# Performance work log

Hardware: AMD Instinct MI355X
Metric: run time of the kernel (lower is better)

Reference implementation:

```python
import jax, jax.numpy as jnp
import numpy as np

B, L, T, D, H, DH = 8, 1024, 1024, 768, 12, 64
SPATIAL_DIM = 5


def setup_inputs() -> dict:
    key = jax.random.key(0)
    ks = jax.random.split(key, 12)
    scale = 1.0 / np.sqrt(D)
    inp = {
        "q": jax.random.normal(ks[0], (B, L, D), dtype=jnp.float32),
        "k": jax.random.normal(ks[1], (B, T, D), dtype=jnp.float32),
        "v": jax.random.normal(ks[2], (B, T, D), dtype=jnp.float32),
        "pairwise_locs": jax.random.normal(ks[3], (B, L, T, SPATIAL_DIM), dtype=jnp.float32),
        # last 64 key positions are padding in every batch row (never all-True)
        "key_padding_mask": jnp.broadcast_to(jnp.arange(T) >= T - 64, (B, T)),
        "Wq": jax.random.normal(ks[4], (D, H * DH), dtype=jnp.float32) * scale,
        "bq": jnp.zeros((H * DH,), dtype=jnp.float32),
        "Wk": jax.random.normal(ks[5], (D, H * DH), dtype=jnp.float32) * scale,
        "bk": jnp.zeros((H * DH,), dtype=jnp.float32),
        "Wv": jax.random.normal(ks[6], (D, H * DH), dtype=jnp.float32) * scale,
        "bv": jnp.zeros((H * DH,), dtype=jnp.float32),
        "Wo": jax.random.normal(ks[7], (H * DH, D), dtype=jnp.float32) * scale,
        "bo": jnp.zeros((D,), dtype=jnp.float32),
    }
    return inp


def reference(q, k, v, pairwise_locs, key_padding_mask, Wq, bq, Wk, bk, Wv, bv, Wo, bo):
    # pairwise_locs is accepted but unused in this forward path (as in the source).
    b, l, _ = q.shape
    t = k.shape[1]
    qh = (q @ Wq + bq).reshape(b, l, H, DH)  # b l h d
    kh = (k @ Wk + bk).reshape(b, t, H, DH)  # b t h d
    vh = (v @ Wv + bv).reshape(b, t, H, DH)  # b t h d
    attn = jnp.einsum('blhd,bthd->bhlt', qh, kh) / jnp.sqrt(jnp.float32(DH))
    attn = jnp.where(key_padding_mask[:, None, None, :], -jnp.inf, attn)
    fused_attn = jax.nn.softmax(attn, axis=-1)
    out = jnp.einsum('bhlt,bthd->blhd', fused_attn, vh).reshape(b, l, H * DH)
    return out @ Wo + bo  # dropout is identity in eval mode
```

## Files before the change

kernel.cpp:

```cpp
#include <hip/hip_runtime.h>
#include <hip/hip_bf16.h>
#include <cstdint>
#include <cstddef>

#define NB 8
#define NL 1024
#define NT 1024
#define ND 768
#define NH 12
#define NDH 64
#define NM (NB*NL)

typedef short short8 __attribute__((ext_vector_type(8)));
typedef unsigned short ushort4v __attribute__((ext_vector_type(4)));
typedef unsigned int uint4v __attribute__((ext_vector_type(4)));
typedef float f32x4 __attribute__((ext_vector_type(4)));
typedef float float4v __attribute__((ext_vector_type(4)));

__device__ __forceinline__ unsigned short f2bf(float f) {
  union { __hip_bfloat16 h; unsigned short u; } cv;
  cv.h = __float2bfloat16(f);
  return cv.u;
}
__device__ __forceinline__ unsigned pk2(float lo, float hi) {
  return (unsigned)f2bf(lo) | ((unsigned)f2bf(hi) << 16);
}
__device__ __forceinline__ void gll16(const void* g, void* l) {
  __builtin_amdgcn_global_load_lds(
      (const __attribute__((address_space(1))) unsigned int*)g,
      (__attribute__((address_space(3))) unsigned int*)l, 16, 0, 0);
}

__global__ __launch_bounds__(256) void cvt_kernel(
    const float* __restrict__ q, const float* __restrict__ k,
    const float* __restrict__ v, unsigned short* __restrict__ qb,
    unsigned short* __restrict__ kb, unsigned short* __restrict__ vb) {
  const float* src = blockIdx.y == 0 ? q : blockIdx.y == 1 ? k : v;
  unsigned short* dst = blockIdx.y == 0 ? qb : blockIdx.y == 1 ? kb : vb;
  size_t i = ((size_t)blockIdx.x * 256 + threadIdx.x) * 8;
  float4v x0 = *(const float4v*)&src[i];
  float4v x1 = *(const float4v*)&src[i + 4];
  uint4v y = {pk2(x0[0], x0[1]), pk2(x0[2], x0[3]),
              pk2(x1[0], x1[1]), pk2(x1[2], x1[3])};
  *(uint4v*)&dst[i] = y;
}

__global__ __launch_bounds__(256) void wt_kernel(
    const float* __restrict__ W0, const float* __restrict__ W1,
    const float* __restrict__ W2, const float* __restrict__ W3,
    unsigned short* __restrict__ Wt) {
  __shared__ float tile[32][33];
  const float* W = blockIdx.z == 0 ? W0 : blockIdx.z == 1 ? W1 : blockIdx.z == 2 ? W2 : W3;
  const int k0 = blockIdx.x * 32, n0 = blockIdx.y * 32;
  const int tx = threadIdx.x & 31, ty = threadIdx.x >> 5;
  for (int r = ty; r < 32; r += 8) tile[r][tx] = W[(size_t)(k0 + r) * ND + n0 + tx];
  __syncthreads();
  unsigned short* out = Wt + (size_t)blockIdx.z * ND * ND;
  for (int r = ty; r < 32; r += 8) out[(size_t)(n0 + r) * ND + k0 + tx] = f2bf(tile[tx][r]);
}

template<int MODE>
__global__ __launch_bounds__(256) void gemm_kernel(
    const unsigned short* __restrict__ A0, const unsigned short* __restrict__ A1,
    const unsigned short* __restrict__ Wt,
    const float* __restrict__ bias0, const float* __restrict__ bias1,
    unsigned short* __restrict__ outb0, unsigned short* __restrict__ outb1,
    float* __restrict__ outf) {
  __shared__ __align__(16) unsigned short As[128 * 64];
  __shared__ __align__(16) unsigned short Bs[128 * 64];
  const int tid = threadIdx.x, lane = tid & 63, w = tid >> 6;
  const int c = lane & 15, g = lane >> 4;
  const int wrow = w & 1, wcol = w >> 1;
  const int l8 = lane >> 3, l7 = lane & 7, csw = l7 ^ l8;
  const int mbase = blockIdx.x * 128, nbase = blockIdx.y * 128;
  const int z = (MODE == 0) ? blockIdx.z : MODE;

  const unsigned short* A = (MODE == 0) ? (z == 0 ? A0 : A1) : A0;
  const unsigned short* Bt = Wt + (size_t)z * ND * ND;
  const float* bias = (MODE == 0) ? (z == 0 ? bias0 : bias1) : bias0;

  f32x4 acc[4][4];
#pragma unroll
  for (int m = 0; m < 4; m++)
#pragma unroll
    for (int n = 0; n < 4; n++) acc[m][n] = (f32x4){0.f, 0.f, 0.f, 0.f};

  for (int k0 = 0; k0 < ND; k0 += 64) {
#pragma unroll
    for (int it = 0; it < 4; it++) {
      int r = it * 32 + w * 8 + l8;
      gll16(&A[(size_t)(mbase + r) * ND + k0 + csw * 8], &As[(it * 32 + w * 8) * 64]);
      gll16(&Bt[(size_t)(nbase + r) * ND + k0 + csw * 8], &Bs[(it * 32 + w * 8) * 64]);
    }
    __syncthreads();

#pragma unroll
    for (int ks = 0; ks < 2; ks++) {
      short8 a[4], b[4];
#pragma unroll
      for (int m = 0; m < 4; m++) {
        int r = wrow * 64 + m * 16 + c;
        a[m] = *(const short8*)&As[r * 64 + (((ks * 4 + g) ^ (c & 7)) * 8)];
      }
#pragma unroll
      for (int n = 0; n < 4; n++) {
        int r = wcol * 64 + n * 16 + c;
        b[n] = *(const short8*)&Bs[r * 64 + (((ks * 4 + g) ^ (c & 7)) * 8)];
      }
#pragma unroll
      for (int m = 0; m < 4; m++)
#pragma unroll
        for (int n = 0; n < 4; n++) {
          if (MODE == 2)
            acc[m][n] = __builtin_amdgcn_mfma_f32_16x16x32_bf16(a[m], b[n], acc[m][n], 0, 0, 0);
          else
            acc[m][n] = __builtin_amdgcn_mfma_f32_16x16x32_bf16(b[n], a[m], acc[m][n], 0, 0, 0);
        }
    }
    __syncthreads();
  }

  if (MODE == 2) {
#pragma unroll
    for (int n = 0; n < 4; n++) {
      const int col = nbase + wcol * 64 + n * 16 + c;
      const float bv = bias[col];
      const int h = col >> 6, dd = col & 63;
#pragma unroll
      for (int m = 0; m < 4; m++) {
        const int r0 = mbase + wrow * 64 + m * 16 + g * 4;
        const int bb = r0 >> 10, t = r0 & (NT - 1);
        ushort4v y;
#pragma unroll
        for (int j = 0; j < 4; j++) y[j] = f2bf(acc[m][n][j] + bv);
        *(ushort4v*)&outb0[((size_t)(bb * NH + h) * NDH + dd) * NT + t] = y;
      }
    }
  } else {
    const float scale = (MODE == 0 && z == 0) ? 0.125f : 1.0f;
    unsigned short* outb = (MODE == 0) ? (z == 0 ? outb0 : outb1) : nullptr;
#pragma unroll
    for (int n = 0; n < 4; n++) {
      const int colb = nbase + wcol * 64 + n * 16 + g * 4;
      float4v bv4 = *(const float4v*)&bias[colb];
#pragma unroll
      for (int m = 0; m < 4; m++) {
        const int row = mbase + wrow * 64 + m * 16 + c;
        if (MODE == 3) {
          float4v y;
#pragma unroll
          for (int j = 0; j < 4; j++) y[j] = acc[m][n][j] + bv4[j];
          *(float4v*)&outf[(size_t)row * ND + colb] = y;
        } else {
          ushort4v y;
#pragma unroll
          for (int j = 0; j < 4; j++) y[j] = f2bf((acc[m][n][j] + bv4[j]) * scale);
          *(ushort4v*)&outb[(size_t)row * ND + colb] = y;
        }
      }
    }
  }
}

__global__ __launch_bounds__(256) void attn_kernel(
    const unsigned short* __restrict__ qh, const unsigned short* __restrict__ kh,
    const unsigned short* __restrict__ vhT, const unsigned int* __restrict__ mask,
    unsigned short* __restrict__ ao) {
  __shared__ __align__(16) unsigned short Ks[2][64 * 64];
  __shared__ __align__(16) unsigned short Vs[2][64 * 64];
  __shared__ __align__(16) unsigned short Ps[4][32][72];
  const int tid = threadIdx.x, lane = tid & 63, w = tid >> 6;
  const int c = lane & 15, g = lane >> 4;
  const int l8 = lane >> 3, l7 = lane & 7, csw = l7 ^ l8;
  const int qb = blockIdx.x * 128;
  const int b = blockIdx.y / NH, h = blockIdx.y % NH;
  const size_t kbase = (size_t)b * NT * ND + h * NDH;
  const size_t vbase = (size_t)(b * NH + h) * NDH * NT;

  short8 aq[2][2];
#pragma unroll
  for (int half = 0; half < 2; half++) {
    size_t qrow = (size_t)(b * NL + qb + w * 32 + half * 16 + c) * ND + h * NDH;
#pragma unroll
    for (int ks = 0; ks < 2; ks++)
      aq[half][ks] = *(const short8*)&qh[qrow + ks * 32 + g * 8];
  }

  f32x4 o[2][4];
#pragma unroll
  for (int half = 0; half < 2; half++)
#pragma unroll
    for (int f = 0; f < 4; f++) o[half][f] = (f32x4){0.f, 0.f, 0.f, 0.f};
  float mr[2] = {-1e30f, -1e30f}, lr[2] = {0.f, 0.f};

#pragma unroll
  for (int it = 0; it < 2; it++) {
    int r = w * 16 + it * 8 + l8;
    gll16(&kh[kbase + (size_t)r * ND + csw * 8], &Ks[0][(w * 16 + it * 8) * 64]);
    gll16(&vhT[vbase + (size_t)r * NT + csw * 8], &Vs[0][(w * 16 + it * 8) * 64]);
  }
  __syncthreads();

  for (int t0 = 0; t0 < NT; t0 += 64) {
    const int cur = (t0 >> 6) & 1;
    if (t0 + 64 < NT) {
#pragma unroll
      for (int it = 0; it < 2; it++) {
        int r = w * 16 + it * 8 + l8;
        gll16(&kh[kbase + (size_t)(t0 + 64 + r) * ND + csw * 8],
              &Ks[cur ^ 1][(w * 16 + it * 8) * 64]);
        gll16(&vhT[vbase + (size_t)r * NT + (t0 + 64) + csw * 8],
              &Vs[cur ^ 1][(w * 16 + it * 8) * 64]);
      }
    }

    f32x4 s[2][4];
#pragma unroll
    for (int half = 0; half < 2; half++)
#pragma unroll
      for (int n = 0; n < 4; n++) s[half][n] = (f32x4){0.f, 0.f, 0.f, 0.f};
    __builtin_amdgcn_s_setprio(1);
#pragma unroll
    for (int ks = 0; ks < 2; ks++)
#pragma unroll
      for (int n = 0; n < 4; n++) {
        short8 ak = *(const short8*)&Ks[cur][(n * 16 + c) * 64 + (((ks * 4 + g) ^ (c & 7)) * 8)];
        s[0][n] = __builtin_amdgcn_mfma_f32_16x16x32_bf16(ak, aq[0][ks], s[0][n], 0, 0, 0);
        s[1][n] = __builtin_amdgcn_mfma_f32_16x16x32_bf16(ak, aq[1][ks], s[1][n], 0, 0, 0);
      }
    __builtin_amdgcn_s_setprio(0);

    {
      uint4v mm[4];
      unsigned any = 0;
#pragma unroll
      for (int n = 0; n < 4; n++) {
        mm[n] = *(const uint4v*)&mask[(size_t)b * NT + t0 + n * 16 + g * 4];
        any |= mm[n][0] | mm[n][1] | mm[n][2] | mm[n][3];
      }
      if (__any(any != 0u)) {
#pragma unroll
        for (int n = 0; n < 4; n++)
#pragma unroll
          for (int j = 0; j < 4; j++)
            if (mm[n][j]) { s[0][n][j] = -INFINITY; s[1][n][j] = -INFINITY; }
      }
    }

#pragma unroll
    for (int half = 0; half < 2; half++) {
      float m01 = fmaxf(fmaxf(s[half][0][0], s[half][0][1]), fmaxf(s[half][0][2], s[half][0][3]));
      float m23 = fmaxf(fmaxf(s[half][1][0], s[half][1][1]), fmaxf(s[half][1][2], s[half][1][3]));
      float m45 = fmaxf(fmaxf(s[half][2][0], s[half][2][1]), fmaxf(s[half][2][2], s[half][2][3]));
      float m67 = fmaxf(fmaxf(s[half][3][0], s[half][3][1]), fmaxf(s[half][3][2], s[half][3][3]));
      float mt = fmaxf(fmaxf(m01, m23), fmaxf(m45, m67));
      mt = fmaxf(mt, __shfl_xor(mt, 16, 64));
      mt = fmaxf(mt, __shfl_xor(mt, 32, 64));
      if (!__all(mt <= mr[half] + 8.f)) {
        float mnew = fmaxf(mr[half], mt);
        float alpha = __expf(mr[half] - mnew);
        lr[half] *= alpha;
#pragma unroll
        for (int f = 0; f < 4; f++)
#pragma unroll
          for (int j = 0; j < 4; j++) o[half][f][j] *= alpha;
        mr[half] = mnew;
      }
      float rs = 0.f;
#pragma unroll
      for (int n = 0; n < 4; n++)
#pragma unroll
        for (int j = 0; j < 4; j++) {
          float p = __expf(s[half][n][j] - mr[half]);
          s[half][n][j] = p;
          rs += p;
        }
      rs += __shfl_xor(rs, 16, 64);
      rs += __shfl_xor(rs, 32, 64);
      lr[half] += rs;
      unsigned* pr = (unsigned*)&Ps[w][half * 16 + c][0];
#pragma unroll
      for (int n = 0; n < 4; n++) {
        pr[n * 8 + g * 2]     = pk2(s[half][n][0], s[half][n][1]);
        pr[n * 8 + g * 2 + 1] = pk2(s[half][n][2], s[half][n][3]);
      }
    }

    __builtin_amdgcn_s_setprio(1);
#pragma unroll
    for (int ks = 0; ks < 2; ks++) {
      short8 bp0 = *(const short8*)&Ps[w][c][ks * 32 + g * 8];
      short8 bp1 = *(const short8*)&Ps[w][16 + c][ks * 32 + g * 8];
#pragma unroll
      for (int f = 0; f < 4; f++) {
        short8 av = *(const short8*)&Vs[cur][(f * 16 + c) * 64 + (((ks * 4 + g) ^ (c & 7)) * 8)];
        o[0][f] = __builtin_amdgcn_mfma_f32_16x16x32_bf16(av, bp0, o[0][f], 0, 0, 0);
        o[1][f] = __builtin_amdgcn_mfma_f32_16x16x32_bf16(av, bp1, o[1][f], 0, 0, 0);
      }
    }
    __builtin_amdgcn_s_setprio(0);
    __syncthreads();
  }

#pragma unroll
  for (int half = 0; half < 2; half++) {
    float inv = 1.f / lr[half];
    size_t row = (size_t)(b * NL + qb + w * 32 + half * 16 + c) * ND + h * NDH;
#pragma unroll
    for (int f = 0; f < 4; f++) {
      ushort4v y;
#pragma unroll
      for (int j = 0; j < 4; j++) y[j] = f2bf(o[half][f][j] * inv);
      *(ushort4v*)&ao[row + f * 16 + g * 4] = y;
    }
  }
}

extern "C" void kernel_launch(void* const* d_in, const int* in_sizes, int n_in,
                              void* d_out, int out_size, void* d_ws, size_t ws_size,
                              hipStream_t stream) {
  const float* q  = (const float*)d_in[0];
  const float* k  = (const float*)d_in[1];
  const float* v  = (const float*)d_in[2];
  const unsigned int* mask = (const unsigned int*)d_in[4];
  const float* Wq = (const float*)d_in[5];
  const float* bq = (const float*)d_in[6];
  const float* Wk = (const float*)d_in[7];
  const float* bk = (const float*)d_in[8];
  const float* Wv = (const float*)d_in[9];
  const float* bv = (const float*)d_in[10];
  const float* Wo = (const float*)d_in[11];
  const float* bo = (const float*)d_in[12];
  float* out = (float*)d_out;

  unsigned short* ws  = (unsigned short*)d_ws;
  unsigned short* Wt  = ws;
  unsigned short* qb  = Wt + (size_t)4 * ND * ND;
  unsigned short* kb  = qb + (size_t)NM * ND;
  unsigned short* vb  = kb + (size_t)NM * ND;
  unsigned short* qhb = vb + (size_t)NM * ND;
  unsigned short* khb = qhb + (size_t)NM * ND;
  unsigned short* vhT = khb + (size_t)NM * ND;
  unsigned short* aob = vhT + (size_t)NM * ND;

  wt_kernel<<<dim3(ND / 32, ND / 32, 4), 256, 0, stream>>>(Wq, Wk, Wv, Wo, Wt);
  cvt_kernel<<<dim3(NM * ND / 8 / 256, 3), 256, 0, stream>>>(q, k, v, qb, kb, vb);

  gemm_kernel<0><<<dim3(NM / 128, ND / 128, 2), 256, 0, stream>>>(
      qb, kb, Wt, bq, bk, qhb, khb, nullptr);
  gemm_kernel<2><<<dim3(NM / 128, ND / 128), 256, 0, stream>>>(
      vb, nullptr, Wt, bv, nullptr, vhT, nullptr, nullptr);

  attn_kernel<<<dim3(NL / 128, NB * NH), 256, 0, stream>>>(qhb, khb, vhT, mask, aob);

  gemm_kernel<3><<<dim3(NM / 128, ND / 128), 256, 0, stream>>>(
      aob, nullptr, Wt, bo, nullptr, nullptr, nullptr, out);
}
```

Baseline: 168.9 us.

## Fuse fp32-to-bf16 input conversion into projection GEMMs and use exp2 softmax

Drops the separate conversion kernel. The Q/K/V projection GEMMs now stream fp32 activations straight into LDS with a swizzled layout and convert them to bf16 on each fragment read. This removes a full write-and-reread of three bf16 activation copies, at the cost of double-size A tiles in LDS (64KB total) and repeated conversion work per N-tile. It also folds log2(e) into the query scale so the softmax can use exp2f instead of __expf.

```diff
diff --git a/kernel.cpp b/kernel.cpp
--- a/kernel.cpp
+++ b/kernel.cpp
@@ -2,6 +2,7 @@
 #include <hip/hip_bf16.h>
 #include <cstdint>
 #include <cstddef>
+#include <cmath>
 
 #define NB 8
 #define NL 1024
@@ -25,24 +26,16 @@
 __device__ __forceinline__ unsigned pk2(float lo, float hi) {
   return (unsigned)f2bf(lo) | ((unsigned)f2bf(hi) << 16);
 }
+__device__ __forceinline__ short8 cvt8(float4v x0, float4v x1) {
+  union { short8 s; uint4v u; } r;
+  r.u = (uint4v){pk2(x0[0], x0[1]), pk2(x0[2], x0[3]),
+                 pk2(x1[0], x1[1]), pk2(x1[2], x1[3])};
+  return r.s;
+}
 __device__ __forceinline__ void gll16(const void* g, void* l) {
   __builtin_amdgcn_global_load_lds(
       (const __attribute__((address_space(1))) unsigned int*)g,
       (__attribute__((address_space(3))) unsigned int*)l, 16, 0, 0);
-}
-
-__global__ __launch_bounds__(256) void cvt_kernel(
-    const float* __restrict__ q, const float* __restrict__ k,
-    const float* __restrict__ v, unsigned short* __restrict__ qb,
-    unsigned short* __restrict__ kb, unsigned short* __restrict__ vb) {
-  const float* src = blockIdx.y == 0 ? q : blockIdx.y == 1 ? k : v;
-  unsigned short* dst = blockIdx.y == 0 ? qb : blockIdx.y == 1 ? kb : vb;
-  size_t i = ((size_t)blockIdx.x * 256 + threadIdx.x) * 8;
-  float4v x0 = *(const float4v*)&src[i];
-  float4v x1 = *(const float4v*)&src[i + 4];
-  uint4v y = {pk2(x0[0], x0[1]), pk2(x0[2], x0[3]),
-              pk2(x1[0], x1[1]), pk2(x1[2], x1[3])};
-  *(uint4v*)&dst[i] = y;
 }
 
 __global__ __launch_bounds__(256) void wt_kernel(
@@ -61,12 +54,13 @@
 
 template<int MODE>
 __global__ __launch_bounds__(256) void gemm_kernel(
-    const unsigned short* __restrict__ A0, const unsigned short* __restrict__ A1,
-    const unsigned short* __restrict__ Wt,
+    const float* __restrict__ Af0, const float* __restrict__ Af1,
+    const unsigned short* __restrict__ Ab, const unsigned short* __restrict__ Wt,
     const float* __restrict__ bias0, const float* __restrict__ bias1,
     unsigned short* __restrict__ outb0, unsigned short* __restrict__ outb1,
     float* __restrict__ outf) {
-  __shared__ __align__(16) unsigned short As[128 * 64];
+  constexpr bool AF32 = (MODE != 3);
+  __shared__ __align__(16) unsigned char AsRaw[AF32 ? 128 * 64 * 4 : 128 * 64 * 2];
   __shared__ __align__(16) unsigned short Bs[128 * 64];
   const int tid = threadIdx.x, lane = tid & 63, w = tid >> 6;
   const int c = lane & 15, g = lane >> 4;
@@ -75,9 +69,9 @@
   const int mbase = blockIdx.x * 128, nbase = blockIdx.y * 128;
   const int z = (MODE == 0) ? blockIdx.z : MODE;
 
-  const unsigned short* A = (MODE == 0) ? (z == 0 ? A0 : A1) : A0;
+  const float* Af = AF32 ? ((MODE == 0 && z == 1) ? Af1 : Af0) : nullptr;
   const unsigned short* Bt = Wt + (size_t)z * ND * ND;
-  const float* bias = (MODE == 0) ? (z == 0 ? bias0 : bias1) : bias0;
+  const float* bias = (MODE == 0 && z == 1) ? bias1 : bias0;
 
   f32x4 acc[4][4];
 #pragma unroll
@@ -86,10 +80,26 @@
     for (int n = 0; n < 4; n++) acc[m][n] = (f32x4){0.f, 0.f, 0.f, 0.f};
 
   for (int k0 = 0; k0 < ND; k0 += 64) {
+    if (AF32) {
+      float* Asf = (float*)AsRaw;
+#pragma unroll
+      for (int it = 0; it < 8; it++) {
+        int r0 = it * 16 + w * 4;
+        int r = r0 + (lane >> 4);
+        int gc = (lane & 15) ^ (r & 15);
+        gll16(&Af[(size_t)(mbase + r) * ND + k0 + gc * 4], &Asf[r0 * 64]);
+      }
+    } else {
+      unsigned short* Asb = (unsigned short*)AsRaw;
+#pragma unroll
+      for (int it = 0; it < 4; it++) {
+        int r = it * 32 + w * 8 + l8;
+        gll16(&Ab[(size_t)(mbase + r) * ND + k0 + csw * 8], &Asb[(it * 32 + w * 8) * 64]);
+      }
+    }
 #pragma unroll
     for (int it = 0; it < 4; it++) {
       int r = it * 32 + w * 8 + l8;
-      gll16(&A[(size_t)(mbase + r) * ND + k0 + csw * 8], &As[(it * 32 + w * 8) * 64]);
       gll16(&Bt[(size_t)(nbase + r) * ND + k0 + csw * 8], &Bs[(it * 32 + w * 8) * 64]);
     }
     __syncthreads();
@@ -100,7 +110,16 @@
 #pragma unroll
       for (int m = 0; m < 4; m++) {
         int r = wrow * 64 + m * 16 + c;
-        a[m] = *(const short8*)&As[r * 64 + (((ks * 4 + g) ^ (c & 7)) * 8)];
+        if (AF32) {
+          const float* Asf = (const float*)AsRaw;
+          int cc = ks * 8 + g * 2;
+          float4v x0 = *(const float4v*)&Asf[r * 64 + ((cc ^ (r & 15)) * 4)];
+          float4v x1 = *(const float4v*)&Asf[r * 64 + (((cc + 1) ^ (r & 15)) * 4)];
+          a[m] = cvt8(x0, x1);
+        } else {
+          const unsigned short* Asb = (const unsigned short*)AsRaw;
+          a[m] = *(const short8*)&Asb[r * 64 + (((ks * 4 + g) ^ (c & 7)) * 8)];
+        }
       }
 #pragma unroll
       for (int n = 0; n < 4; n++) {
@@ -137,7 +156,7 @@
       }
     }
   } else {
-    const float scale = (MODE == 0 && z == 0) ? 0.125f : 1.0f;
+    const float scale = (MODE == 0 && z == 0) ? 0.125f * 1.44269504f : 1.0f;
     unsigned short* outb = (MODE == 0) ? (z == 0 ? outb0 : outb1) : nullptr;
 #pragma unroll
     for (int n = 0; n < 4; n++) {
@@ -258,7 +277,7 @@
       mt = fmaxf(mt, __shfl_xor(mt, 32, 64));
       if (!__all(mt <= mr[half] + 8.f)) {
         float mnew = fmaxf(mr[half], mt);
-        float alpha = __expf(mr[half] - mnew);
+        float alpha = exp2f(mr[half] - mnew);
         lr[half] *= alpha;
 #pragma unroll
         for (int f = 0; f < 4; f++)
@@ -271,7 +290,7 @@
       for (int n = 0; n < 4; n++)
 #pragma unroll
         for (int j = 0; j < 4; j++) {
-          float p = __expf(s[half][n][j] - mr[half]);
+          float p = exp2f(s[half][n][j] - mr[half]);
           s[half][n][j] = p;
           rs += p;
         }
@@ -335,24 +354,20 @@
 
   unsigned short* ws  = (unsigned short*)d_ws;
   unsigned short* Wt  = ws;
-  unsigned short* qb  = Wt + (size_t)4 * ND * ND;
-  unsigned short* kb  = qb + (size_t)NM * ND;
-  unsigned short* vb  = kb + (size_t)NM * ND;
-  unsigned short* qhb = vb + (size_t)NM * ND;
+  unsigned short* qhb = Wt + (size_t)4 * ND * ND;
   unsigned short* khb = qhb + (size_t)NM * ND;
   unsigned short* vhT = khb + (size_t)NM * ND;
   unsigned short* aob = vhT + (size_t)NM * ND;
 
   wt_kernel<<<dim3(ND / 32, ND / 32, 4), 256, 0, stream>>>(Wq, Wk, Wv, Wo, Wt);
-  cvt_kernel<<<dim3(NM * ND / 8 / 256, 3), 256, 0, stream>>>(q, k, v, qb, kb, vb);
 
   gemm_kernel<0><<<dim3(NM / 128, ND / 128, 2), 256, 0, stream>>>(
-      qb, kb, Wt, bq, bk, qhb, khb, nullptr);
+      q, k, nullptr, Wt, bq, bk, qhb, khb, nullptr);
   gemm_kernel<2><<<dim3(NM / 128, ND / 128), 256, 0, stream>>>(
-      vb, nullptr, Wt, bv, nullptr, vhT, nullptr, nullptr);
+      v, nullptr, nullptr, Wt, bv, nullptr, vhT, nullptr, nullptr);
 
   attn_kernel<<<dim3(NL / 128, NB * NH), 256, 0, stream>>>(qhb, khb, vhT, mask, aob);
 
   gemm_kernel<3><<<dim3(NM / 128, ND / 128), 256, 0, stream>>>(
-      aob, nullptr, Wt, bo, nullptr, nullptr, nullptr, out);
-}
+      nullptr, nullptr, aob, Wt, bo, nullptr, nullptr, nullptr, out);
+}
```

New measurement: 172.6 us. +2.2%, slower.
